# Optimization experiments

Measured on AMD Instinct MI355X. Metric: run time of the kernel, lower is better.

## Reference

```python
import jax, jax.numpy as jnp
import numpy as np

K = 16                 # neighbors
CH = (64, 64, 64)      # edge-MLP channels
C_IN = 64              # input feature channels
EPS = 1e-3             # Keras BatchNormalization default epsilon


def setup_inputs() -> dict:
    key = jax.random.key(0)
    ks = jax.random.split(key, 24)
    B, N = 256, 128
    inp = {}
    inp["points"] = jax.random.normal(ks[0], (B, N, 2), jnp.float32)
    inp["features"] = jax.random.normal(ks[1], (B, N, C_IN), jnp.float32)
    ins = [2 * C_IN, CH[0], CH[1]]
    i = 2
    for l, (cin, cout) in enumerate(zip(ins, CH)):
        inp[f"w{l}"] = jax.random.normal(ks[i], (cin, cout), jnp.float32) / np.sqrt(cin).astype(np.float32); i += 1
        inp[f"g{l}"] = jnp.ones((cout,), jnp.float32)
        inp[f"b{l}"] = jnp.zeros((cout,), jnp.float32)
        inp[f"m{l}"] = 0.1 * jax.random.normal(ks[i], (cout,), jnp.float32); i += 1
        inp[f"v{l}"] = jnp.ones((cout,), jnp.float32)
    inp["wsc"] = jax.random.normal(ks[i], (C_IN, CH[-1]), jnp.float32) / np.sqrt(C_IN).astype(np.float32); i += 1
    inp["gsc"] = jnp.ones((CH[-1],), jnp.float32)
    inp["bsc"] = jnp.zeros((CH[-1],), jnp.float32)
    inp["msc"] = 0.1 * jax.random.normal(ks[i], (CH[-1],), jnp.float32)
    inp["vsc"] = jnp.ones((CH[-1],), jnp.float32)
    return inp


def _bn(x, g, b, m, v):
    # inference-mode BatchNorm over last (channel) axis
    return (x - m) * jax.lax.rsqrt(v + EPS) * g + b


def _forward(points, features, params):
    # pairwise squared distances  [B, N, N]
    r = jnp.sum(points * points, axis=-1, keepdims=True)
    d = r - 2.0 * jnp.einsum('bnd,bmd->bnm', points, points) + jnp.swapaxes(r, 1, 2)
    # k+1 nearest (incl. self), drop self  -> [B, N, K]
    _, idx = jax.lax.top_k(-d, K + 1)
    idx = idx[:, :, 1:]
    # gather neighbor features  [B, N, K, C]
    knn = jax.vmap(lambda f, i: f[i])(features, idx)
    center = features[:, :, None, :]
    # edge features: concat(center, neighbor - center)  [B, N, K, 2C]
    x = jnp.concatenate([jnp.broadcast_to(center, knn.shape), knn - center], axis=-1)
    # edge MLP: 1x1 convs == per-edge matmuls
    for (w, g, b, m, v) in params[:-1]:
        x = jax.nn.relu(_bn(jnp.einsum('bnkc,cd->bnkd', x, w), g, b, m, v))
    pooled = jnp.mean(x, axis=2)                      # [B, N, C_out]
    wsc, gsc, bsc, msc, vsc = params[-1]
    sc = _bn(features @ wsc, gsc, bsc, msc, vsc)      # shortcut 1x1 conv + BN
    return jax.nn.relu(sc + pooled)


def reference(points, features,
              w0, g0, b0, m0, v0,
              w1, g1, b1, m1, v1,
              w2, g2, b2, m2, v2,
              wsc, gsc, bsc, msc, vsc):
    params = [(w0, g0, b0, m0, v0), (w1, g1, b1, m1, v1),
              (w2, g2, b2, m2, v2), (wsc, gsc, bsc, msc, vsc)]
    return _forward(points, features, params)
```

## Files before the change

kernel.cpp:

```cpp
#include <hip/hip_runtime.h>
#include <stdint.h>


#define KK 16
#define EPSV 1e-3f
#define SW0 136
#define SW 72

typedef __bf16 bf16x8 __attribute__((ext_vector_type(8)));
typedef float f32x4 __attribute__((ext_vector_type(4)));
union B8 { uint4 u; bf16x8 v; };

__device__ __forceinline__ unsigned int f2ord(float f) {
  unsigned int u = __float_as_uint(f);
  return (u & 0x80000000u) ? ~u : (u | 0x80000000u);
}
__device__ __forceinline__ unsigned short f2bs(float f) {
  __bf16 b = (__bf16)f;
  return __builtin_bit_cast(unsigned short, b);
}
__device__ __forceinline__ unsigned int pk(float lo, float hi) {
  return (unsigned int)f2bs(lo) | ((unsigned int)f2bs(hi) << 16);
}

__global__ __launch_bounds__(256) void knn_kernel(const float* __restrict__ pts,
                                                  int* __restrict__ knn) {
  __shared__ __align__(16) unsigned long long keys[4][128];
  const int wv = threadIdx.x >> 6;
  const int lane = threadIdx.x & 63;
  const int row = blockIdx.x * 4 + wv;
  const int b = row >> 7;
  const int n = row & 127;
  const float2* pb = (const float2*)(pts + b * 128 * 2);
  const float2 pn = pb[n];
  const float rn = __fadd_rn(__fmul_rn(pn.x, pn.x), __fmul_rn(pn.y, pn.y));

  unsigned long long key0, key1;
#pragma unroll
  for (int h = 0; h < 2; ++h) {
    const int j = lane + h * 64;
    const float2 pj = pb[j];
    const float rj = __fadd_rn(__fmul_rn(pj.x, pj.x), __fmul_rn(pj.y, pj.y));
    const float dot = __fadd_rn(__fmul_rn(pn.x, pj.x), __fmul_rn(pn.y, pj.y));
    const float d = __fadd_rn(__fsub_rn(rn, __fmul_rn(2.0f, dot)), rj);
    unsigned long long k = ((unsigned long long)f2ord(d) << 32) | (unsigned int)j;
    if (h == 0) key0 = k; else key1 = k;
  }
  keys[wv][lane] = key0;
  keys[wv][lane + 64] = key1;
  int c0 = 0, c1 = 0;
#pragma unroll 8
  for (int j = 0; j < 128; j += 2) {
    const ulonglong2 kp = *(const ulonglong2*)&keys[wv][j];
    c0 += (kp.x < key0); c0 += (kp.y < key0);
    c1 += (kp.x < key1); c1 += (kp.y < key1);
  }
  if (c0 >= 1 && c0 <= 16) knn[row * KK + c0 - 1] = lane;
  if (c1 >= 1 && c1 <= 16) knn[row * KK + c1 - 1] = lane + 64;
}

__global__ __launch_bounds__(256, 2) void mlp_kernel(
    const float* __restrict__ feat, const int* __restrict__ knnIdx,
    const float* __restrict__ w0, const float* __restrict__ g0,
    const float* __restrict__ b0, const float* __restrict__ m0,
    const float* __restrict__ v0, const float* __restrict__ w1,
    const float* __restrict__ g1, const float* __restrict__ b1,
    const float* __restrict__ m1, const float* __restrict__ v1,
    const float* __restrict__ w2, const float* __restrict__ g2,
    const float* __restrict__ b2, const float* __restrict__ m2,
    const float* __restrict__ v2, const float* __restrict__ wsc,
    const float* __restrict__ gsc, const float* __restrict__ bsc,
    const float* __restrict__ msc, const float* __restrict__ vsc,
    float* __restrict__ out) {
  __shared__ __align__(16) unsigned short w0T[64 * SW0];
  __shared__ __align__(16) unsigned short w1T[64 * SW];
  __shared__ __align__(16) unsigned short w2T[64 * SW];
  __shared__ __align__(16) unsigned short wscT[64 * SW];
  __shared__ __align__(16) unsigned short X0[4][16 * SW];

  const int tid = threadIdx.x;
  const int wv = tid >> 6;
  const int lane = tid & 63;
  const int m = lane & 15;
  const int q4 = lane >> 4;

#pragma unroll
  for (int q = 0; q < 8; ++q) {
    const int v = tid + 256 * q;
    const float4 w = ((const float4*)w0)[v];
    const int i = v >> 4, c = (v & 15) << 2;
    w0T[(c + 0) * SW0 + i] = f2bs(w.x);
    w0T[(c + 1) * SW0 + i] = f2bs(w.y);
    w0T[(c + 2) * SW0 + i] = f2bs(w.z);
    w0T[(c + 3) * SW0 + i] = f2bs(w.w);
  }
#pragma unroll
  for (int q = 0; q < 4; ++q) {
    const int v = tid + 256 * q;
    const int i = v >> 4, c = (v & 15) << 2;
    float4 w = ((const float4*)w1)[v];
    w1T[(c + 0) * SW + i] = f2bs(w.x);
    w1T[(c + 1) * SW + i] = f2bs(w.y);
    w1T[(c + 2) * SW + i] = f2bs(w.z);
    w1T[(c + 3) * SW + i] = f2bs(w.w);
    w = ((const float4*)w2)[v];
    w2T[(c + 0) * SW + i] = f2bs(w.x);
    w2T[(c + 1) * SW + i] = f2bs(w.y);
    w2T[(c + 2) * SW + i] = f2bs(w.z);
    w2T[(c + 3) * SW + i] = f2bs(w.w);
    w = ((const float4*)wsc)[v];
    wscT[(c + 0) * SW + i] = f2bs(w.x);
    wscT[(c + 1) * SW + i] = f2bs(w.y);
    wscT[(c + 2) * SW + i] = f2bs(w.z);
    wscT[(c + 3) * SW + i] = f2bs(w.w);
  }

  float s0[4], o0[4], s1[4], o1[4], s2[4], o2[4], ssc[4], osc[4];
#pragma unroll
  for (int nt = 0; nt < 4; ++nt) {
    const int c = nt * 16 + m;
    float s;
    s = g0[c] / sqrtf(v0[c] + EPSV); s0[nt] = s; o0[nt] = b0[c] - m0[c] * s;
    s = g1[c] / sqrtf(v1[c] + EPSV); s1[nt] = s; o1[nt] = b1[c] - m1[c] * s;
    s = g2[c] / sqrtf(v2[c] + EPSV); s2[nt] = s; o2[nt] = b2[c] - m2[c] * s;
    s = gsc[c] / sqrtf(vsc[c] + EPSV); ssc[nt] = s; osc[nt] = bsc[c] - msc[c] * s;
  }

  const int row0 = blockIdx.x * 64 + wv * 16;
  const int kk = lane >> 2, pp = lane & 3;

  int jdx[16];
#pragma unroll
  for (int rr = 0; rr < 16; ++rr) jdx[rr] = knnIdx[(row0 + rr) * KK + kk];

  {
    const int r = lane >> 2, p = lane & 3;
    const float4* fr = (const float4*)(feat + (row0 + r) * 64);
    const float4 a = fr[p * 4 + 0], bq = fr[p * 4 + 1];
    const float4 cq = fr[p * 4 + 2], dq = fr[p * 4 + 3];
    uint4 u0, u1;
    u0.x = pk(a.x, a.y); u0.y = pk(a.z, a.w);
    u0.z = pk(bq.x, bq.y); u0.w = pk(bq.z, bq.w);
    u1.x = pk(cq.x, cq.y); u1.y = pk(cq.z, cq.w);
    u1.z = pk(dq.x, dq.y); u1.w = pk(dq.z, dq.w);
    *(uint4*)&X0[wv][r * SW + p * 16] = u0;
    *(uint4*)&X0[wv][r * SW + p * 16 + 8] = u1;
  }

  const float* featb = feat + (row0 >> 7) * (128 * 64);
  float4 n0, n1, n2, n3;
  {
    const float4* np_ = (const float4*)(featb + jdx[0] * 64);
    n0 = np_[pp * 4 + 0]; n1 = np_[pp * 4 + 1];
    n2 = np_[pp * 4 + 2]; n3 = np_[pp * 4 + 3];
  }

  __syncthreads();

  const f32x4 fzero = {0.f, 0.f, 0.f, 0.f};
  f32x4 sacc[4] = {fzero, fzero, fzero, fzero};
  f32x4 ctp[4] = {fzero, fzero, fzero, fzero};
  f32x4 cbt[4] = {fzero, fzero, fzero, fzero};
#pragma unroll
  for (int t = 0; t < 2; ++t) {
    B8 af; af.u = *(const uint4*)&X0[wv][m * SW + t * 32 + q4 * 8];
#pragma unroll
    for (int nt = 0; nt < 4; ++nt) {
      B8 bs, bt, bb;
      bs.u = *(const uint4*)&wscT[(nt * 16 + m) * SW + t * 32 + q4 * 8];
      bt.u = *(const uint4*)&w0T[(nt * 16 + m) * SW0 + t * 32 + q4 * 8];
      bb.u = *(const uint4*)&w0T[(nt * 16 + m) * SW0 + 64 + t * 32 + q4 * 8];
      sacc[nt] = __builtin_amdgcn_mfma_f32_16x16x32_bf16(af.v, bs.v, sacc[nt], 0, 0, 0);
      ctp[nt]  = __builtin_amdgcn_mfma_f32_16x16x32_bf16(af.v, bt.v, ctp[nt], 0, 0, 0);
      cbt[nt]  = __builtin_amdgcn_mfma_f32_16x16x32_bf16(af.v, bb.v, cbt[nt], 0, 0, 0);
    }
  }
  float scf[4][4], ct[4][4];
#pragma unroll
  for (int nt = 0; nt < 4; ++nt)
#pragma unroll
    for (int r = 0; r < 4; ++r) {
      scf[nt][r] = fmaf(sacc[nt][r], ssc[nt], osc[nt]);
      ct[nt][r] = ctp[nt][r] - cbt[nt][r];
    }

#pragma unroll
  for (int rr = 0; rr < 16; ++rr) {
    const int qo = rr >> 2, ri = rr & 3;
    const int row = row0 + rr;

    {
      uint4 u;
      u.x = pk(n0.x, n0.y); u.y = pk(n0.z, n0.w);
      u.z = pk(n1.x, n1.y); u.w = pk(n1.z, n1.w);
      *(uint4*)&X0[wv][kk * SW + pp * 16] = u;
      u.x = pk(n2.x, n2.y); u.y = pk(n2.z, n2.w);
      u.z = pk(n3.x, n3.y); u.w = pk(n3.z, n3.w);
      *(uint4*)&X0[wv][kk * SW + pp * 16 + 8] = u;
    }
    if (rr < 15) {
      const float4* np_ = (const float4*)(featb + jdx[rr + 1] * 64);
      n0 = np_[pp * 4 + 0]; n1 = np_[pp * 4 + 1];
      n2 = np_[pp * 4 + 2]; n3 = np_[pp * 4 + 3];
    }

    f32x4 acc[4];
#pragma unroll
    for (int nt = 0; nt < 4; ++nt) {
      const float ci = __shfl(ct[nt][ri], qo * 16 + m);
      f32x4 a; a[0] = ci; a[1] = ci; a[2] = ci; a[3] = ci;
      acc[nt] = a;
    }
#pragma unroll
    for (int t = 0; t < 2; ++t) {
      B8 af; af.u = *(const uint4*)&X0[wv][m * SW + t * 32 + q4 * 8];
#pragma unroll
      for (int nt = 0; nt < 4; ++nt) {
        B8 bf_; bf_.u = *(const uint4*)&w0T[(nt * 16 + m) * SW0 + 64 + t * 32 + q4 * 8];
        acc[nt] = __builtin_amdgcn_mfma_f32_16x16x32_bf16(af.v, bf_.v, acc[nt], 0, 0, 0);
      }
    }
#pragma unroll
    for (int nt = 0; nt < 4; ++nt)
#pragma unroll
      for (int r2 = 0; r2 < 4; ++r2) {
        const float y = fmaxf(fmaf(acc[nt][r2], s0[nt], o0[nt]), 0.f);
        X0[wv][(q4 * 4 + r2) * SW + nt * 16 + m] = f2bs(y);
      }

    acc[0] = fzero; acc[1] = fzero; acc[2] = fzero; acc[3] = fzero;
#pragma unroll
    for (int t = 0; t < 2; ++t) {
      B8 af; af.u = *(const uint4*)&X0[wv][m * SW + t * 32 + q4 * 8];
#pragma unroll
      for (int nt = 0; nt < 4; ++nt) {
        B8 bf_; bf_.u = *(const uint4*)&w1T[(nt * 16 + m) * SW + t * 32 + q4 * 8];
        acc[nt] = __builtin_amdgcn_mfma_f32_16x16x32_bf16(af.v, bf_.v, acc[nt], 0, 0, 0);
      }
    }
#pragma unroll
    for (int nt = 0; nt < 4; ++nt)
#pragma unroll
      for (int r2 = 0; r2 < 4; ++r2) {
        const float y = fmaxf(fmaf(acc[nt][r2], s1[nt], o1[nt]), 0.f);
        X0[wv][(q4 * 4 + r2) * SW + nt * 16 + m] = f2bs(y);
      }

    acc[0] = fzero; acc[1] = fzero; acc[2] = fzero; acc[3] = fzero;
#pragma unroll
    for (int t = 0; t < 2; ++t) {
      B8 af; af.u = *(const uint4*)&X0[wv][m * SW + t * 32 + q4 * 8];
#pragma unroll
      for (int nt = 0; nt < 4; ++nt) {
        B8 bf_; bf_.u = *(const uint4*)&w2T[(nt * 16 + m) * SW + t * 32 + q4 * 8];
        acc[nt] = __builtin_amdgcn_mfma_f32_16x16x32_bf16(af.v, bf_.v, acc[nt], 0, 0, 0);
      }
    }

    float pool[4];
#pragma unroll
    for (int nt = 0; nt < 4; ++nt) {
      float p_ = 0.f;
#pragma unroll
      for (int r2 = 0; r2 < 4; ++r2)
        p_ += fmaxf(fmaf(acc[nt][r2], s2[nt], o2[nt]), 0.f);
      p_ += __shfl_xor(p_, 16);
      p_ += __shfl_xor(p_, 32);
      pool[nt] = p_ * 0.0625f;
    }
    if (q4 == qo) {
#pragma unroll
      for (int nt = 0; nt < 4; ++nt)
        out[row * 64 + nt * 16 + m] = fmaxf(scf[nt][ri] + pool[nt], 0.f);
    }
  }
}

extern "C" void kernel_launch(void* const* d_in, const int* in_sizes, int n_in,
                              void* d_out, int out_size, void* d_ws, size_t ws_size,
                              hipStream_t stream) {
  const float* pts = (const float*)d_in[0];
  const float* feat = (const float*)d_in[1];
  const float* w0 = (const float*)d_in[2];
  const float* g0 = (const float*)d_in[3];
  const float* b0 = (const float*)d_in[4];
  const float* m0 = (const float*)d_in[5];
  const float* v0 = (const float*)d_in[6];
  const float* w1 = (const float*)d_in[7];
  const float* g1 = (const float*)d_in[8];
  const float* b1 = (const float*)d_in[9];
  const float* m1 = (const float*)d_in[10];
  const float* v1 = (const float*)d_in[11];
  const float* w2 = (const float*)d_in[12];
  const float* g2 = (const float*)d_in[13];
  const float* b2 = (const float*)d_in[14];
  const float* m2 = (const float*)d_in[15];
  const float* v2 = (const float*)d_in[16];
  const float* wsc = (const float*)d_in[17];
  const float* gsc = (const float*)d_in[18];
  const float* bsc = (const float*)d_in[19];
  const float* msc = (const float*)d_in[20];
  const float* vsc = (const float*)d_in[21];
  float* out = (float*)d_out;

  int* knn = (int*)d_ws;

  knn_kernel<<<dim3(256 * 128 / 4), dim3(256), 0, stream>>>(pts, knn);
  mlp_kernel<<<dim3(512), dim3(256), 0, stream>>>(
      feat, knn, w0, g0, b0, m0, v0, w1, g1, b1, m1, v1, w2, g2, b2, m2, v2,
      wsc, gsc, bsc, msc, vsc, out);
}
```

Measured before the change: 171.8 us.

## Process two rows per iteration with double-buffered LDS tiles for MFMA interleaving

Restructures the per-row edge-MLP loop to handle two query rows at once. Each wave gets two LDS staging buffers, and the independent MFMA chains for both rows are interleaved to hide MFMA latency and LDS round-trips. Neighbor features for the next pair are now gathered and packed to bf16 one iteration ahead. The launch-bounds occupancy hint is dropped, which allows more registers per thread at the risk of lower occupancy, and LDS use grows by the second buffer.

```diff
diff --git a/kernel.cpp b/kernel.cpp
--- a/kernel.cpp
+++ b/kernel.cpp
@@ -59,7 +59,7 @@
   if (c1 >= 1 && c1 <= 16) knn[row * KK + c1 - 1] = lane + 64;
 }
 
-__global__ __launch_bounds__(256, 2) void mlp_kernel(
+__global__ __launch_bounds__(256) void mlp_kernel(
     const float* __restrict__ feat, const int* __restrict__ knnIdx,
     const float* __restrict__ w0, const float* __restrict__ g0,
     const float* __restrict__ b0, const float* __restrict__ m0,
@@ -76,7 +76,7 @@
   __shared__ __align__(16) unsigned short w1T[64 * SW];
   __shared__ __align__(16) unsigned short w2T[64 * SW];
   __shared__ __align__(16) unsigned short wscT[64 * SW];
-  __shared__ __align__(16) unsigned short X0[4][16 * SW];
+  __shared__ __align__(16) unsigned short X0[4][2][16 * SW];
 
   const int tid = threadIdx.x;
   const int wv = tid >> 6;
@@ -143,16 +143,30 @@
     u0.z = pk(bq.x, bq.y); u0.w = pk(bq.z, bq.w);
     u1.x = pk(cq.x, cq.y); u1.y = pk(cq.z, cq.w);
     u1.z = pk(dq.x, dq.y); u1.w = pk(dq.z, dq.w);
-    *(uint4*)&X0[wv][r * SW + p * 16] = u0;
-    *(uint4*)&X0[wv][r * SW + p * 16 + 8] = u1;
+    *(uint4*)&X0[wv][0][r * SW + p * 16] = u0;
+    *(uint4*)&X0[wv][0][r * SW + p * 16 + 8] = u1;
   }
 
   const float* featb = feat + (row0 >> 7) * (128 * 64);
-  float4 n0, n1, n2, n3;
+
+  uint4 uA0, uA1, uB0, uB1;
   {
     const float4* np_ = (const float4*)(featb + jdx[0] * 64);
-    n0 = np_[pp * 4 + 0]; n1 = np_[pp * 4 + 1];
-    n2 = np_[pp * 4 + 2]; n3 = np_[pp * 4 + 3];
+    const float4 n0 = np_[pp * 4 + 0], n1 = np_[pp * 4 + 1];
+    const float4 n2 = np_[pp * 4 + 2], n3 = np_[pp * 4 + 3];
+    uA0.x = pk(n0.x, n0.y); uA0.y = pk(n0.z, n0.w);
+    uA0.z = pk(n1.x, n1.y); uA0.w = pk(n1.z, n1.w);
+    uA1.x = pk(n2.x, n2.y); uA1.y = pk(n2.z, n2.w);
+    uA1.z = pk(n3.x, n3.y); uA1.w = pk(n3.z, n3.w);
+  }
+  {
+    const float4* np_ = (const float4*)(featb + jdx[1] * 64);
+    const float4 n0 = np_[pp * 4 + 0], n1 = np_[pp * 4 + 1];
+    const float4 n2 = np_[pp * 4 + 2], n3 = np_[pp * 4 + 3];
+    uB0.x = pk(n0.x, n0.y); uB0.y = pk(n0.z, n0.w);
+    uB0.z = pk(n1.x, n1.y); uB0.w = pk(n1.z, n1.w);
+    uB1.x = pk(n2.x, n2.y); uB1.y = pk(n2.z, n2.w);
+    uB1.z = pk(n3.x, n3.y); uB1.w = pk(n3.z, n3.w);
   }
 
   __syncthreads();
@@ -163,7 +177,7 @@
   f32x4 cbt[4] = {fzero, fzero, fzero, fzero};
 #pragma unroll
   for (int t = 0; t < 2; ++t) {
-    B8 af; af.u = *(const uint4*)&X0[wv][m * SW + t * 32 + q4 * 8];
+    B8 af; af.u = *(const uint4*)&X0[wv][0][m * SW + t * 32 + q4 * 8];
 #pragma unroll
     for (int nt = 0; nt < 4; ++nt) {
       B8 bs, bt, bb;
@@ -185,93 +199,130 @@
     }
 
 #pragma unroll
-  for (int rr = 0; rr < 16; ++rr) {
-    const int qo = rr >> 2, ri = rr & 3;
-    const int row = row0 + rr;
-
-    {
-      uint4 u;
-      u.x = pk(n0.x, n0.y); u.y = pk(n0.z, n0.w);
-      u.z = pk(n1.x, n1.y); u.w = pk(n1.z, n1.w);
-      *(uint4*)&X0[wv][kk * SW + pp * 16] = u;
-      u.x = pk(n2.x, n2.y); u.y = pk(n2.z, n2.w);
-      u.z = pk(n3.x, n3.y); u.w = pk(n3.z, n3.w);
-      *(uint4*)&X0[wv][kk * SW + pp * 16 + 8] = u;
-    }
-    if (rr < 15) {
-      const float4* np_ = (const float4*)(featb + jdx[rr + 1] * 64);
-      n0 = np_[pp * 4 + 0]; n1 = np_[pp * 4 + 1];
-      n2 = np_[pp * 4 + 2]; n3 = np_[pp * 4 + 3];
-    }
-
-    f32x4 acc[4];
+  for (int rp = 0; rp < 8; ++rp) {
+    const int qo = rp >> 1;
+    const int riA = (2 * rp) & 3, riB = (2 * rp + 1) & 3;
+    const int rowA = row0 + 2 * rp, rowB = rowA + 1;
+
+    *(uint4*)&X0[wv][0][kk * SW + pp * 16] = uA0;
+    *(uint4*)&X0[wv][0][kk * SW + pp * 16 + 8] = uA1;
+    *(uint4*)&X0[wv][1][kk * SW + pp * 16] = uB0;
+    *(uint4*)&X0[wv][1][kk * SW + pp * 16 + 8] = uB1;
+
+    if (rp < 7) {
+      {
+        const float4* np_ = (const float4*)(featb + jdx[2 * rp + 2] * 64);
+        const float4 n0 = np_[pp * 4 + 0], n1 = np_[pp * 4 + 1];
+        const float4 n2 = np_[pp * 4 + 2], n3 = np_[pp * 4 + 3];
+        uA0.x = pk(n0.x, n0.y); uA0.y = pk(n0.z, n0.w);
+        uA0.z = pk(n1.x, n1.y); uA0.w = pk(n1.z, n1.w);
+        uA1.x = pk(n2.x, n2.y); uA1.y = pk(n2.z, n2.w);
+        uA1.z = pk(n3.x, n3.y); uA1.w = pk(n3.z, n3.w);
+      }
+      {
+        const float4* np_ = (const float4*)(featb + jdx[2 * rp + 3] * 64);
+        const float4 n0 = np_[pp * 4 + 0], n1 = np_[pp * 4 + 1];
+        const float4 n2 = np_[pp * 4 + 2], n3 = np_[pp * 4 + 3];
+        uB0.x = pk(n0.x, n0.y); uB0.y = pk(n0.z, n0.w);
+        uB0.z = pk(n1.x, n1.y); uB0.w = pk(n1.z, n1.w);
+        uB1.x = pk(n2.x, n2.y); uB1.y = pk(n2.z, n2.w);
+        uB1.z = pk(n3.x, n3.y); uB1.w = pk(n3.z, n3.w);
+      }
+    }
+
+    f32x4 accA[4], accB[4];
 #pragma unroll
     for (int nt = 0; nt < 4; ++nt) {
-      const float ci = __shfl(ct[nt][ri], qo * 16 + m);
-      f32x4 a; a[0] = ci; a[1] = ci; a[2] = ci; a[3] = ci;
-      acc[nt] = a;
+      const float cA = __shfl(ct[nt][riA], qo * 16 + m);
+      const float cB = __shfl(ct[nt][riB], qo * 16 + m);
+      f32x4 a; a[0] = cA; a[1] = cA; a[2] = cA; a[3] = cA;
+      accA[nt] = a;
+      f32x4 b; b[0] = cB; b[1] = cB; b[2] = cB; b[3] = cB;
+      accB[nt] = b;
     }
 #pragma unroll
     for (int t = 0; t < 2; ++t) {
-      B8 af; af.u = *(const uint4*)&X0[wv][m * SW + t * 32 + q4 * 8];
+      B8 afA, afB;
+      afA.u = *(const uint4*)&X0[wv][0][m * SW + t * 32 + q4 * 8];
+      afB.u = *(const uint4*)&X0[wv][1][m * SW + t * 32 + q4 * 8];
 #pragma unroll
       for (int nt = 0; nt < 4; ++nt) {
         B8 bf_; bf_.u = *(const uint4*)&w0T[(nt * 16 + m) * SW0 + 64 + t * 32 + q4 * 8];
-        acc[nt] = __builtin_amdgcn_mfma_f32_16x16x32_bf16(af.v, bf_.v, acc[nt], 0, 0, 0);
+        accA[nt] = __builtin_amdgcn_mfma_f32_16x16x32_bf16(afA.v, bf_.v, accA[nt], 0, 0, 0);
+        accB[nt] = __builtin_amdgcn_mfma_f32_16x16x32_bf16(afB.v, bf_.v, accB[nt], 0, 0, 0);
       }
     }
 #pragma unroll
     for (int nt = 0; nt < 4; ++nt)
 #pragma unroll
       for (int r2 = 0; r2 < 4; ++r2) {
-        const float y = fmaxf(fmaf(acc[nt][r2], s0[nt], o0[nt]), 0.f);
-        X0[wv][(q4 * 4 + r2) * SW + nt * 16 + m] = f2bs(y);
-      }
-
-    acc[0] = fzero; acc[1] = fzero; acc[2] = fzero; acc[3] = fzero;
+        const float yA = fmaxf(fmaf(accA[nt][r2], s0[nt], o0[nt]), 0.f);
+        const float yB = fmaxf(fmaf(accB[nt][r2], s0[nt], o0[nt]), 0.f);
+        X0[wv][0][(q4 * 4 + r2) * SW + nt * 16 + m] = f2bs(yA);
+        X0[wv][1][(q4 * 4 + r2) * SW + nt * 16 + m] = f2bs(yB);
+      }
+
+#pragma unroll
+    for (int nt = 0; nt < 4; ++nt) { accA[nt] = fzero; accB[nt] = fzero; }
 #pragma unroll
     for (int t = 0; t < 2; ++t) {
-      B8 af; af.u = *(const uint4*)&X0[wv][m * SW + t * 32 + q4 * 8];
+      B8 afA, afB;
+      afA.u = *(const uint4*)&X0[wv][0][m * SW + t * 32 + q4 * 8];
+      afB.u = *(const uint4*)&X0[wv][1][m * SW + t * 32 + q4 * 8];
 #pragma unroll
       for (int nt = 0; nt < 4; ++nt) {
         B8 bf_; bf_.u = *(const uint4*)&w1T[(nt * 16 + m) * SW + t * 32 + q4 * 8];
-        acc[nt] = __builtin_amdgcn_mfma_f32_16x16x32_bf16(af.v, bf_.v, acc[nt], 0, 0, 0);
+        accA[nt] = __builtin_amdgcn_mfma_f32_16x16x32_bf16(afA.v, bf_.v, accA[nt], 0, 0, 0);
+        accB[nt] = __builtin_amdgcn_mfma_f32_16x16x32_bf16(afB.v, bf_.v, accB[nt], 0, 0, 0);
       }
     }
 #pragma unroll
     for (int nt = 0; nt < 4; ++nt)
 #pragma unroll
       for (int r2 = 0; r2 < 4; ++r2) {
-        const float y = fmaxf(fmaf(acc[nt][r2], s1[nt], o1[nt]), 0.f);
-        X0[wv][(q4 * 4 + r2) * SW + nt * 16 + m] = f2bs(y);
-      }
-
-    acc[0] = fzero; acc[1] = fzero; acc[2] = fzero; acc[3] = fzero;
+        const float yA = fmaxf(fmaf(accA[nt][r2], s1[nt], o1[nt]), 0.f);
+        const float yB = fmaxf(fmaf(accB[nt][r2], s1[nt], o1[nt]), 0.f);
+        X0[wv][0][(q4 * 4 + r2) * SW + nt * 16 + m] = f2bs(yA);
+        X0[wv][1][(q4 * 4 + r2) * SW + nt * 16 + m] = f2bs(yB);
+      }
+
+#pragma unroll
+    for (int nt = 0; nt < 4; ++nt) { accA[nt] = fzero; accB[nt] = fzero; }
 #pragma unroll
     for (int t = 0; t < 2; ++t) {
-      B8 af; af.u = *(const uint4*)&X0[wv][m * SW + t * 32 + q4 * 8];
+      B8 afA, afB;
+      afA.u = *(const uint4*)&X0[wv][0][m * SW + t * 32 + q4 * 8];
+      afB.u = *(const uint4*)&X0[wv][1][m * SW + t * 32 + q4 * 8];
 #pragma unroll
       for (int nt = 0; nt < 4; ++nt) {
         B8 bf_; bf_.u = *(const uint4*)&w2T[(nt * 16 + m) * SW + t * 32 + q4 * 8];
-        acc[nt] = __builtin_amdgcn_mfma_f32_16x16x32_bf16(af.v, bf_.v, acc[nt], 0, 0, 0);
-      }
-    }
-
-    float pool[4];
+        accA[nt] = __builtin_amdgcn_mfma_f32_16x16x32_bf16(afA.v, bf_.v, accA[nt], 0, 0, 0);
+        accB[nt] = __builtin_amdgcn_mfma_f32_16x16x32_bf16(afB.v, bf_.v, accB[nt], 0, 0, 0);
+      }
+    }
+
+    float poolA[4], poolB[4];
 #pragma unroll
     for (int nt = 0; nt < 4; ++nt) {
-      float p_ = 0.f;
-#pragma unroll
-      for (int r2 = 0; r2 < 4; ++r2)
-        p_ += fmaxf(fmaf(acc[nt][r2], s2[nt], o2[nt]), 0.f);
-      p_ += __shfl_xor(p_, 16);
-      p_ += __shfl_xor(p_, 32);
-      pool[nt] = p_ * 0.0625f;
+      float pa = 0.f, pb2 = 0.f;
+#pragma unroll
+      for (int r2 = 0; r2 < 4; ++r2) {
+        pa += fmaxf(fmaf(accA[nt][r2], s2[nt], o2[nt]), 0.f);
+        pb2 += fmaxf(fmaf(accB[nt][r2], s2[nt], o2[nt]), 0.f);
+      }
+      pa += __shfl_xor(pa, 16);
+      pa += __shfl_xor(pa, 32);
+      poolA[nt] = pa * 0.0625f;
+      pb2 += __shfl_xor(pb2, 16);
+      pb2 += __shfl_xor(pb2, 32);
+      poolB[nt] = pb2 * 0.0625f;
     }
     if (q4 == qo) {
 #pragma unroll
-      for (int nt = 0; nt < 4; ++nt)
-        out[row * 64 + nt * 16 + m] = fmaxf(scf[nt][ri] + pool[nt], 0.f);
+      for (int nt = 0; nt < 4; ++nt) {
+        out[rowA * 64 + nt * 16 + m] = fmaxf(scf[nt][riA] + poolA[nt], 0.f);
+        out[rowB * 64 + nt * 16 + m] = fmaxf(scf[nt][riB] + poolB[nt], 0.f);
+      }
     }
   }
 }
```

Result: no change. 171.0 us, median of 2 (-0.5%).
